# Optimization experiments

Hardware: AMD Instinct MI355X
Metric: run time of the kernel (lower is better)

## Reference

```python
import jax, jax.numpy as jnp
import numpy as np

B, C, N_MAX = 32, 1, 1024
HID, CLS, ATT_E, ATT_H = 128, 64, 64, 128
D = HID + CLS            # node_state_dim = hidden + class_repr
EDGE_F = 2 * ATT_E       # 128
K_MIX = 20
N_GNN = B * C * N_MAX    # 32768 GNN nodes
N_FEAT = N_GNN + 1       # node_feat rows after zero-pad row
E = 200_000
E_OUT = 500_000
NUM_SUB = 1024
NUM_PROP = 2             # num_GNN_prop (num_GNN_layers = 1)


def _lin(k, din, dout):
    k1, k2 = jax.random.split(k)
    s = 1.0 / np.sqrt(din)
    return (jax.random.uniform(k1, (din, dout), minval=-s, maxval=s),
            jax.random.uniform(k2, (dout,), minval=-s, maxval=s))


def setup_inputs() -> dict:
    key = jax.random.key(0)
    ks = jax.random.split(key, 30)
    inp = {}
    inp['A_pad'] = (jax.random.uniform(ks[0], (B, C, N_MAX, N_MAX)) < 0.05).astype(jnp.float32)
    inp['edges'] = jax.random.randint(ks[1], (E, 2), 0, N_GNN)
    inp['att_idx'] = jax.random.randint(ks[2], (N_GNN,), 0, ATT_E)
    inp['node_idx_feat'] = jax.random.randint(ks[3], (N_GNN,), 0, N_FEAT)
    inp['class_label'] = jax.random.randint(ks[4], (N_GNN,), 0, 2)
    inp['node_idx_gnn'] = jax.random.randint(ks[5], (E_OUT, 2), 0, N_GNN)
    inp['label'] = (jax.random.uniform(ks[6], (E_OUT,)) < 0.3).astype(jnp.float32)
    inp['subgraph_idx'] = jax.random.randint(ks[7], (E_OUT,), 0, NUM_SUB)
    # learned parameters
    inp['W_dec'], inp['b_dec'] = _lin(ks[8], N_MAX, HID)
    inp['class_emb'] = jax.random.normal(ks[9], (2, CLS)) * 0.1
    inp['W_msg1'], inp['b_msg1'] = _lin(ks[10], D + EDGE_F, D)
    inp['W_msg2'], inp['b_msg2'] = _lin(ks[11], D, D)
    inp['W_att1'], inp['b_att1'] = _lin(ks[12], D + EDGE_F, ATT_H)
    inp['W_att2'], inp['b_att2'] = _lin(ks[13], ATT_H, D)
    inp['W_ih'], inp['b_ih'] = _lin(ks[14], D, 3 * D)
    inp['W_hh'], inp['b_hh'] = _lin(ks[15], D, 3 * D)
    inp['Wt1'], inp['bt1'] = _lin(ks[16], D, HID)
    inp['Wt2'], inp['bt2'] = _lin(ks[17], HID, HID)
    inp['Wt3'], inp['bt3'] = _lin(ks[18], HID, K_MIX)
    inp['Wa1'], inp['ba1'] = _lin(ks[19], D, HID)
    inp['Wa2'], inp['ba2'] = _lin(ks[20], HID, HID)
    inp['Wa3'], inp['ba3'] = _lin(ks[21], HID, K_MIX)
    return inp


def _gran_forward(A_pad, label, W_dec, b_dec, class_emb,
                  W_msg1, b_msg1, W_msg2, b_msg2, W_att1, b_att1, W_att2, b_att2,
                  W_ih, b_ih, W_hh, b_hh, Wt1, bt1, Wt2, bt2, Wt3, bt3,
                  Wa1, ba1, Wa2, ba2, Wa3, ba3,
                  edges, att_idx, node_idx_feat, class_label, node_idx_gnn, subgraph_idx):
    # decoder_input: (B*C*N_max, N_max) -> hidden, then zero-pad one row on top
    A = A_pad.reshape(B * C * N_MAX, N_MAX)
    node_feat = A @ W_dec + b_dec                                   # [N_GNN, HID]
    node_feat = jnp.concatenate([jnp.zeros((1, HID), node_feat.dtype), node_feat], axis=0)
    # att_edge_feat: one-hot(att_idx[src]) || one-hot(att_idx[dst])  (scatter of ones)
    att_edge_feat = jnp.concatenate([
        jax.nn.one_hot(att_idx[edges[:, 0]], ATT_E, dtype=node_feat.dtype),
        jax.nn.one_hot(att_idx[edges[:, 1]], ATT_E, dtype=node_feat.dtype)], axis=1)  # [E, 128]
    # node state = gathered feat ++ class representation
    state = jnp.concatenate([node_feat[node_idx_feat], class_emb[class_label]], axis=1)  # [N_GNN, D]

    src, dst = edges[:, 0], edges[:, 1]

    def prop(state):
        diff = state[src] - state[dst]                              # gather node-diff [E, D]
        ei = jnp.concatenate([diff, att_edge_feat], axis=1)          # [E, D+128]
        msg = jax.nn.relu(ei @ W_msg1 + b_msg1) @ W_msg2 + b_msg2   # edge MLP [E, D]
        att = jax.nn.sigmoid(jax.nn.relu(ei @ W_att1 + b_att1) @ W_att2 + b_att2)
        agg = jax.ops.segment_sum(msg * att, dst, num_segments=N_GNN)  # scatter-add [N_GNN, D]
        # GRUCell(agg, state)
        gi = agg @ W_ih + b_ih
        gh = state @ W_hh + b_hh
        ir, iz, inn = jnp.split(gi, 3, axis=1)
        hr, hz, hn = jnp.split(gh, 3, axis=1)
        r = jax.nn.sigmoid(ir + hr)
        z = jax.nn.sigmoid(iz + hz)
        n = jnp.tanh(inn + r * hn)
        return (1.0 - z) * n + z * state

    for _ in range(NUM_PROP):
        state = prop(state)

    # output edge predictions from state diffs
    dout = state[node_idx_gnn[:, 0]] - state[node_idx_gnn[:, 1]]    # [E_OUT, D]
    h = jax.nn.relu(jax.nn.relu(dout @ Wt1 + bt1) @ Wt2 + bt2)
    log_theta = h @ Wt3 + bt3                                        # [E_OUT, K]
    g = jax.nn.relu(jax.nn.relu(dout @ Wa1 + ba1) @ Wa2 + ba2)
    log_alpha = jax.nn.log_softmax(g @ Wa3 + ba3, axis=1)            # [E_OUT, K]

    # mixture Bernoulli loss (BCEWithLogits, pos_weight=1): softplus(x) - x*y
    adj_loss = jax.nn.softplus(log_theta) - log_theta * label[:, None]
    const = jax.ops.segment_sum(jnp.ones((E_OUT,), log_theta.dtype), subgraph_idx, num_segments=NUM_SUB)
    const = jnp.maximum(const, 1.0)  # guard empty subgraphs with random indices
    red_loss = jax.ops.segment_sum(adj_loss, subgraph_idx, num_segments=NUM_SUB)
    red_alpha = jax.ops.segment_sum(log_alpha, subgraph_idx, num_segments=NUM_SUB) / const[:, None]
    log_prob = jax.nn.logsumexp(-red_loss + red_alpha, axis=1)       # [NUM_SUB]
    return -jnp.sum(log_prob) / float(E_OUT)


def reference(A_pad, edges, att_idx, node_idx_feat, class_label, node_idx_gnn, label, subgraph_idx,
              W_dec, b_dec, class_emb, W_msg1, b_msg1, W_msg2, b_msg2,
              W_att1, b_att1, W_att2, b_att2, W_ih, b_ih, W_hh, b_hh,
              Wt1, bt1, Wt2, bt2, Wt3, bt3, Wa1, ba1, Wa2, ba2, Wa3, ba3):
    return _gran_forward(A_pad, label, W_dec, b_dec, class_emb,
                         W_msg1, b_msg1, W_msg2, b_msg2, W_att1, b_att1, W_att2, b_att2,
                         W_ih, b_ih, W_hh, b_hh, Wt1, bt1, Wt2, bt2, Wt3, bt3,
                         Wa1, ba1, Wa2, ba2, Wa3, ba3,
                         edges, att_idx, node_idx_feat, class_label, node_idx_gnn, subgraph_idx)
```

## Files before the change

kernel.cpp:

```cpp
#include <hip/hip_runtime.h>
#include <math.h>

#define NGNN   32768
#define NMAXD  1024
#define HIDD   128
#define CLSD   64
#define DDIM   192
#define ATTH   128
#define NEDGE  200000
#define NEOUT  500000
#define NSUB   1024
#define KMIX   20

typedef __attribute__((ext_vector_type(8))) short bf16x8;
typedef __attribute__((ext_vector_type(8))) unsigned short u16x8;
typedef __attribute__((ext_vector_type(4))) float f32x4;

__device__ __forceinline__ float sigm(float x) { return 1.0f / (1.0f + __expf(-x)); }
__device__ __forceinline__ float tanhf_(float x) { return 2.0f / (1.0f + __expf(-2.0f * x)) - 1.0f; }

__device__ __forceinline__ short f2bf(float f) {
  union { float f; unsigned u; } v; v.f = f;
  unsigned r = v.u + 0x7FFFu + ((v.u >> 16) & 1u);
  return (short)(r >> 16);
}
__device__ __forceinline__ float bf2f(unsigned short u) {
  union { unsigned u; float f; } v; v.u = ((unsigned)u) << 16;
  return v.f;
}
__device__ __forceinline__ f32x4 bc4(float b) {
  f32x4 v; v[0] = b; v[1] = b; v[2] = b; v[3] = b; return v;
}

__global__ __launch_bounds__(64) void k_pack(const float* __restrict__ W,
                                             short* __restrict__ out, int N, int CT) {
  const int l = threadIdx.x;
  const int ks = blockIdx.x / CT;
  const int ct = blockIdx.x % CT;
  const int row0 = ks * 32 + (l >> 4) * 8;
  const int col = ct * 16 + (l & 15);
  short v[8];
#pragma unroll
  for (int j = 0; j < 8; j++) {
    const float f = (col < N) ? W[(size_t)(row0 + j) * N + col] : 0.0f;
    v[j] = f2bf(f);
  }
  *(bf16x8*)(out + ((size_t)blockIdx.x * 64 + l) * 8) = *(bf16x8*)v;
}

__global__ __launch_bounds__(128) void k_dec(
    const float* __restrict__ A, const float* __restrict__ Wd,
    const float* __restrict__ bd, float* __restrict__ nf) {
  __shared__ float arow[NMAXD];
  __shared__ int   nz[NMAXD];
  __shared__ int   cnt;
  const int row = blockIdx.x;
  const int t = threadIdx.x;
  if (t == 0) cnt = 0;
  const float4* A4 = (const float4*)(A + (size_t)row * NMAXD);
  float4* a4 = (float4*)arow;
  a4[t] = A4[t];
  a4[t + 128] = A4[t + 128];
  __syncthreads();
  for (int i = t; i < NMAXD; i += 128) {
    if (arow[i] != 0.0f) {
      int p = atomicAdd(&cnt, 1);
      nz[p] = i;
    }
  }
  __syncthreads();
  float acc = bd[t];
  const int n = cnt;
  for (int i = 0; i < n; i++) acc += Wd[(size_t)nz[i] * HIDD + t];
  nf[(size_t)row * HIDD + t] = acc;
}

__global__ __launch_bounds__(192) void k_state(
    const float* __restrict__ nf, const float* __restrict__ cemb,
    const int* __restrict__ nif, const int* __restrict__ cl,
    unsigned short* __restrict__ stbf) {
  const int i = blockIdx.x;
  const int t = threadIdx.x;
  float v;
  if (t < HIDD) {
    const int idx = nif[i];
    v = (idx == 0) ? 0.0f : nf[(size_t)(idx - 1) * HIDD + t];
  } else {
    v = cemb[cl[i] * CLSD + (t - HIDD)];
  }
  stbf[(size_t)i * DDIM + t] = (unsigned short)f2bf(v);
}

__global__ __launch_bounds__(128, 4) void k_edge_mfma(
    const unsigned short* __restrict__ stbf, const int* __restrict__ edges,
    const int* __restrict__ attidx,
    const float* __restrict__ Wm1, const float* __restrict__ bm1,
    const short* __restrict__ pWm1, const short* __restrict__ pWm2,
    const float* __restrict__ bm2,
    const float* __restrict__ Wa1, const float* __restrict__ ba1,
    const short* __restrict__ pWa1, const short* __restrict__ pWa2,
    const float* __restrict__ ba2,
    float* __restrict__ agg) {
  __shared__ short phm[6144];
  __shared__ short pha[4096];
  const int t = threadIdx.x;
  const int e0 = blockIdx.x * 32;
  const int wid = t >> 6, l = t & 63;
  const int col16 = l & 15, rr = (l >> 4) * 4;
  const int cb = (l >> 4) * 8;

  bf16x8 dfrag[6];
  {
    const int e = e0 + wid * 16 + (l & 15);
    const int s = edges[2 * e], d = edges[2 * e + 1];
    const unsigned short* ps = &stbf[(size_t)s * DDIM + cb];
    const unsigned short* pd_ = &stbf[(size_t)d * DDIM + cb];
#pragma unroll
    for (int ks = 0; ks < 6; ks++) {
      const u16x8 a = *(const u16x8*)(ps + ks * 32);
      const u16x8 b = *(const u16x8*)(pd_ + ks * 32);
      short v[8];
#pragma unroll
      for (int j = 0; j < 8; j++) v[j] = f2bf(bf2f(a[j]) - bf2f(b[j]));
      dfrag[ks] = *(bf16x8*)v;
    }
  }
  int a0r[4], a1r[4], dstr[4];
#pragma unroll
  for (int j = 0; j < 4; j++) {
    const int e = e0 + wid * 16 + rr + j;
    const int s = edges[2 * e], d = edges[2 * e + 1];
    a0r[j] = attidx[s]; a1r[j] = attidx[d]; dstr[j] = d;
  }

  for (int ct = 0; ct < 12; ct++) {
    const int col = ct * 16 + col16;
    f32x4 acc;
#pragma unroll
    for (int j = 0; j < 4; j++)
      acc[j] = bm1[col] + Wm1[(size_t)(DDIM + a0r[j]) * DDIM + col]
                        + Wm1[(size_t)(DDIM + 64 + a1r[j]) * DDIM + col];
#pragma unroll
    for (int ks = 0; ks < 6; ks++) {
      bf16x8 b = *(const bf16x8*)&pWm1[((ks * 12 + ct) * 64 + l) * 8];
      acc = __builtin_amdgcn_mfma_f32_16x16x32_bf16(dfrag[ks], b, acc, 0, 0, 0);
    }
    const int ksp = col >> 5, gp = (col & 31) >> 3, jp = col & 7;
#pragma unroll
    for (int j = 0; j < 4; j++)
      phm[((wid * 6 + ksp) * 64 + gp * 16 + rr + j) * 8 + jp] = f2bf(fmaxf(acc[j], 0.0f));
  }
  for (int ct = 0; ct < 8; ct++) {
    const int col = ct * 16 + col16;
    f32x4 acc;
#pragma unroll
    for (int j = 0; j < 4; j++)
      acc[j] = ba1[col] + Wa1[(size_t)(DDIM + a0r[j]) * ATTH + col]
                        + Wa1[(size_t)(DDIM + 64 + a1r[j]) * ATTH + col];
#pragma unroll
    for (int ks = 0; ks < 6; ks++) {
      bf16x8 b = *(const bf16x8*)&pWa1[((ks * 8 + ct) * 64 + l) * 8];
      acc = __builtin_amdgcn_mfma_f32_16x16x32_bf16(dfrag[ks], b, acc, 0, 0, 0);
    }
    const int ksp = ct >> 1, gp = ((ct & 1) * 16 + col16) >> 3, jp = col16 & 7;
#pragma unroll
    for (int j = 0; j < 4; j++)
      pha[((wid * 4 + ksp) * 64 + gp * 16 + rr + j) * 8 + jp] = f2bf(fmaxf(acc[j], 0.0f));
  }
  __syncthreads();

  for (int ct = 0; ct < 12; ct++) {
    const int col = ct * 16 + col16;
    f32x4 m = bc4(bm2[col]), av = bc4(ba2[col]);
#pragma unroll
    for (int ks = 0; ks < 6; ks++) {
      bf16x8 a = *(const bf16x8*)&phm[((wid * 6 + ks) * 64 + l) * 8];
      bf16x8 b = *(const bf16x8*)&pWm2[((ks * 12 + ct) * 64 + l) * 8];
      m = __builtin_amdgcn_mfma_f32_16x16x32_bf16(a, b, m, 0, 0, 0);
    }
#pragma unroll
    for (int ks = 0; ks < 4; ks++) {
      bf16x8 a = *(const bf16x8*)&pha[((wid * 4 + ks) * 64 + l) * 8];
      bf16x8 b = *(const bf16x8*)&pWa2[((ks * 12 + ct) * 64 + l) * 8];
      av = __builtin_amdgcn_mfma_f32_16x16x32_bf16(a, b, av, 0, 0, 0);
    }
#pragma unroll
    for (int j = 0; j < 4; j++) {
      atomicAdd(&agg[(size_t)dstr[j] * DDIM + col], m[j] * sigm(av[j]));
    }
  }
}

__global__ __launch_bounds__(256, 2) void k_gru_mfma(
    unsigned short* __restrict__ stbf, const float* __restrict__ agg,
    const short* __restrict__ pWih, const float* __restrict__ bih,
    const short* __restrict__ pWhh, const float* __restrict__ bhh) {
  const int t = threadIdx.x;
  const int n0 = blockIdx.x * 64;
  const int wid = t >> 6, l = t & 63;
  const int col16 = l & 15, rr = (l >> 4) * 4;
  const int cb = (l >> 4) * 8;
  const int row = n0 + wid * 16 + (l & 15);

  bf16x8 af[6], sf[6];
#pragma unroll
  for (int ks = 0; ks < 6; ks++) {
    const float4 a0 = *(const float4*)&agg[(size_t)row * DDIM + ks * 32 + cb];
    const float4 a1 = *(const float4*)&agg[(size_t)row * DDIM + ks * 32 + cb + 4];
    short v[8];
    v[0] = f2bf(a0.x); v[1] = f2bf(a0.y); v[2] = f2bf(a0.z); v[3] = f2bf(a0.w);
    v[4] = f2bf(a1.x); v[5] = f2bf(a1.y); v[6] = f2bf(a1.z); v[7] = f2bf(a1.w);
    af[ks] = *(bf16x8*)v;
    sf[ks] = *(const bf16x8*)&stbf[(size_t)row * DDIM + ks * 32 + cb];
  }

  for (int ct = 0; ct < 12; ct++) {
    const int c = ct * 16 + col16;
    f32x4 ir = bc4(bih[c]), iz = bc4(bih[c + DDIM]), in_ = bc4(bih[c + 2 * DDIM]);
    f32x4 hr = bc4(bhh[c]), hz = bc4(bhh[c + DDIM]), hn = bc4(bhh[c + 2 * DDIM]);
#pragma unroll
    for (int ks = 0; ks < 6; ks++) {
      const bf16x8 wr = *(const bf16x8*)&pWih[((size_t)(ks * 36 + ct) * 64 + l) * 8];
      const bf16x8 wz = *(const bf16x8*)&pWih[((size_t)(ks * 36 + ct + 12) * 64 + l) * 8];
      const bf16x8 wn = *(const bf16x8*)&pWih[((size_t)(ks * 36 + ct + 24) * 64 + l) * 8];
      ir  = __builtin_amdgcn_mfma_f32_16x16x32_bf16(af[ks], wr, ir, 0, 0, 0);
      iz  = __builtin_amdgcn_mfma_f32_16x16x32_bf16(af[ks], wz, iz, 0, 0, 0);
      in_ = __builtin_amdgcn_mfma_f32_16x16x32_bf16(af[ks], wn, in_, 0, 0, 0);
      const bf16x8 vr = *(const bf16x8*)&pWhh[((size_t)(ks * 36 + ct) * 64 + l) * 8];
      const bf16x8 vz = *(const bf16x8*)&pWhh[((size_t)(ks * 36 + ct + 12) * 64 + l) * 8];
      const bf16x8 vn = *(const bf16x8*)&pWhh[((size_t)(ks * 36 + ct + 24) * 64 + l) * 8];
      hr = __builtin_amdgcn_mfma_f32_16x16x32_bf16(sf[ks], vr, hr, 0, 0, 0);
      hz = __builtin_amdgcn_mfma_f32_16x16x32_bf16(sf[ks], vz, hz, 0, 0, 0);
      hn = __builtin_amdgcn_mfma_f32_16x16x32_bf16(sf[ks], vn, hn, 0, 0, 0);
    }
#pragma unroll
    for (int j = 0; j < 4; j++) {
      const size_t idx = (size_t)(n0 + wid * 16 + rr + j) * DDIM + c;
      const float sv = bf2f(stbf[idx]);
      const float r = sigm(ir[j] + hr[j]);
      const float z = sigm(iz[j] + hz[j]);
      const float nn = tanhf_(in_[j] + r * hn[j]);
      stbf[idx] = (unsigned short)f2bf((1.0f - z) * nn + z * sv);
    }
  }
}

__device__ __forceinline__ f32x4 head_branch(
    const bf16x8 dfrag[6], short* ph1, short* ph2,
    const short* __restrict__ pW1, const float* __restrict__ b1,
    const short* __restrict__ pW2, const float* __restrict__ b2,
    const short* __restrict__ pW3, const float* __restrict__ b3,
    int rt, int ch, int l) {
  const int col16 = l & 15, rr = (l >> 4) * 4;
  for (int ci = 0; ci < 4; ci++) {
    const int ct = ch * 4 + ci;
    const int col = ct * 16 + col16;
    f32x4 acc = bc4(b1[col]);
#pragma unroll
    for (int ks = 0; ks < 6; ks++) {
      bf16x8 b = *(const bf16x8*)&pW1[((ks * 8 + ct) * 64 + l) * 8];
      acc = __builtin_amdgcn_mfma_f32_16x16x32_bf16(dfrag[ks], b, acc, 0, 0, 0);
    }
    const int ksp = ct >> 1, gp = ((ct & 1) * 16 + col16) >> 3, jp = col16 & 7;
#pragma unroll
    for (int j = 0; j < 4; j++)
      ph1[((rt * 4 + ksp) * 64 + gp * 16 + rr + j) * 8 + jp] = f2bf(fmaxf(acc[j], 0.0f));
  }
  __syncthreads();
  for (int ci = 0; ci < 4; ci++) {
    const int ct = ch * 4 + ci;
    const int col = ct * 16 + col16;
    f32x4 acc = bc4(b2[col]);
#pragma unroll
    for (int ks = 0; ks < 4; ks++) {
      bf16x8 a = *(const bf16x8*)&ph1[((rt * 4 + ks) * 64 + l) * 8];
      bf16x8 b = *(const bf16x8*)&pW2[((ks * 8 + ct) * 64 + l) * 8];
      acc = __builtin_amdgcn_mfma_f32_16x16x32_bf16(a, b, acc, 0, 0, 0);
    }
    const int ksp = ct >> 1, gp = ((ct & 1) * 16 + col16) >> 3, jp = col16 & 7;
#pragma unroll
    for (int j = 0; j < 4; j++)
      ph2[((rt * 4 + ksp) * 64 + gp * 16 + rr + j) * 8 + jp] = f2bf(fmaxf(acc[j], 0.0f));
  }
  __syncthreads();
  const int col = ch * 16 + col16;
  f32x4 acc = bc4((col < KMIX) ? b3[col] : 0.0f);
#pragma unroll
  for (int ks = 0; ks < 4; ks++) {
    bf16x8 a = *(const bf16x8*)&ph2[((rt * 4 + ks) * 64 + l) * 8];
    bf16x8 b = *(const bf16x8*)&pW3[((ks * 2 + ch) * 64 + l) * 8];
    acc = __builtin_amdgcn_mfma_f32_16x16x32_bf16(a, b, acc, 0, 0, 0);
  }
  return acc;
}

__global__ __launch_bounds__(512, 4) void k_head_mfma(
    const unsigned short* __restrict__ stbf, const int* __restrict__ nig,
    const float* __restrict__ label, const int* __restrict__ subidx,
    const short* __restrict__ pWt1, const float* __restrict__ bt1,
    const short* __restrict__ pWt2, const float* __restrict__ bt2,
    const short* __restrict__ pWt3, const float* __restrict__ bt3,
    const short* __restrict__ pWa1, const float* __restrict__ ba1,
    const short* __restrict__ pWa2, const float* __restrict__ ba2,
    const short* __restrict__ pWa3, const float* __restrict__ ba3,
    float* __restrict__ red_loss, float* __restrict__ red_alpha,
    float* __restrict__ cnt) {
  __shared__ short ph1[8192];
  __shared__ short ph2[8192];
  __shared__ float la[64 * KMIX];
  __shared__ int   ssub[64];
  __shared__ float slab[64];
  __shared__ float lse[64];

  const int t = threadIdx.x;
  const int r0 = blockIdx.x * 64;

  if (t < 64) {
    const int gr = r0 + t;
    const int sb = (gr < NEOUT) ? subidx[gr] : 0;
    ssub[t] = sb;
    slab[t] = (gr < NEOUT) ? label[gr] : 0.0f;
    if (gr < NEOUT) atomicAdd(&cnt[sb], 1.0f);
  }

  const int wid = t >> 6, l = t & 63;
  const int rt = wid & 3, ch = wid >> 2;
  const int col16 = l & 15, rr = (l >> 4) * 4;
  const int cb = (l >> 4) * 8;

  bf16x8 dfrag[6];
  {
    const int gr = r0 + rt * 16 + (l & 15);
    const int ok = (gr < NEOUT);
    const int ia = ok ? nig[2 * gr] : 0;
    const int ib = ok ? nig[2 * gr + 1] : 0;
    const unsigned short* pa = &stbf[(size_t)ia * DDIM + cb];
    const unsigned short* pb = &stbf[(size_t)ib * DDIM + cb];
#pragma unroll
    for (int ks = 0; ks < 6; ks++) {
      const u16x8 a = *(const u16x8*)(pa + ks * 32);
      const u16x8 b = *(const u16x8*)(pb + ks * 32);
      short v[8];
#pragma unroll
      for (int j = 0; j < 8; j++) v[j] = f2bf(bf2f(a[j]) - bf2f(b[j]));
      dfrag[ks] = *(bf16x8*)v;
    }
  }
  __syncthreads();

  {
    const f32x4 o = head_branch(dfrag, ph1, ph2, pWt1, bt1, pWt2, bt2, pWt3, bt3, rt, ch, l);
    const int col = ch * 16 + col16;
    if (col < KMIX) {
#pragma unroll
      for (int j = 0; j < 4; j++) {
        const int r = rt * 16 + rr + j;
        if (r0 + r < NEOUT) {
          const float lt = o[j];
          const float adj = fmaxf(lt, 0.0f) + logf(1.0f + __expf(-fabsf(lt))) - lt * slab[r];
          atomicAdd(&red_loss[ssub[r] * KMIX + col], adj);
        }
      }
    }
  }
  __syncthreads();
  {
    const f32x4 o = head_branch(dfrag, ph1, ph2, pWa1, ba1, pWa2, ba2, pWa3, ba3, rt, ch, l);
    const int col = ch * 16 + col16;
    if (col < KMIX) {
#pragma unroll
      for (int j = 0; j < 4; j++) {
        const int r = rt * 16 + rr + j;
        la[r * KMIX + col] = o[j];
      }
    }
  }
  __syncthreads();
  if (t < 64) {
    float m = -1e30f;
    for (int k = 0; k < KMIX; k++) m = fmaxf(m, la[t * KMIX + k]);
    float s = 0.0f;
    for (int k = 0; k < KMIX; k++) s += __expf(la[t * KMIX + k] - m);
    lse[t] = m + logf(s);
  }
  __syncthreads();
  {
    const int r = t >> 3;
    if (r0 + r < NEOUT) {
#pragma unroll
      for (int i = 0; i < 3; i++) {
        const int c = (t & 7) + 8 * i;
        if (c < KMIX)
          atomicAdd(&red_alpha[ssub[r] * KMIX + c], la[r * KMIX + c] - lse[r]);
      }
    }
  }
}

__global__ __launch_bounds__(1024) void k_final(
    const float* __restrict__ red_loss, const float* __restrict__ red_alpha,
    const float* __restrict__ cnt, float* __restrict__ out) {
  __shared__ float part[1024];
  const int s = threadIdx.x;
  const float c = fmaxf(cnt[s], 1.0f);
  float v[KMIX];
  float m = -1e30f;
  for (int k = 0; k < KMIX; k++) {
    v[k] = -red_loss[s * KMIX + k] + red_alpha[s * KMIX + k] / c;
    m = fmaxf(m, v[k]);
  }
  float sum = 0.0f;
  for (int k = 0; k < KMIX; k++) sum += __expf(v[k] - m);
  part[s] = m + logf(sum);
  __syncthreads();
  for (int st = 512; st > 0; st >>= 1) {
    if (s < st) part[s] += part[s + st];
    __syncthreads();
  }
  if (s == 0) out[0] = -part[0] / (float)NEOUT;
}

extern "C" void kernel_launch(void* const* d_in, const int* in_sizes, int n_in,
                              void* d_out, int out_size, void* d_ws, size_t ws_size,
                              hipStream_t stream) {
  const float* A      = (const float*)d_in[0];
  const int*   edges  = (const int*)d_in[1];
  const int*   attidx = (const int*)d_in[2];
  const int*   nif    = (const int*)d_in[3];
  const int*   cl     = (const int*)d_in[4];
  const int*   nig    = (const int*)d_in[5];
  const float* label  = (const float*)d_in[6];
  const int*   subidx = (const int*)d_in[7];
  const float* Wdec   = (const float*)d_in[8];
  const float* bdec   = (const float*)d_in[9];
  const float* cemb   = (const float*)d_in[10];
  const float* Wm1    = (const float*)d_in[11];
  const float* bm1    = (const float*)d_in[12];
  const float* Wm2    = (const float*)d_in[13];
  const float* bm2    = (const float*)d_in[14];
  const float* Wa1    = (const float*)d_in[15];
  const float* ba1    = (const float*)d_in[16];
  const float* Wa2    = (const float*)d_in[17];
  const float* ba2    = (const float*)d_in[18];
  const float* Wih    = (const float*)d_in[19];
  const float* bih    = (const float*)d_in[20];
  const float* Whh    = (const float*)d_in[21];
  const float* bhh    = (const float*)d_in[22];
  const float* Wt1    = (const float*)d_in[23];
  const float* bt1    = (const float*)d_in[24];
  const float* Wt2    = (const float*)d_in[25];
  const float* bt2    = (const float*)d_in[26];
  const float* Wt3    = (const float*)d_in[27];
  const float* bt3    = (const float*)d_in[28];
  const float* Wha1   = (const float*)d_in[29];
  const float* hba1   = (const float*)d_in[30];
  const float* Wha2   = (const float*)d_in[31];
  const float* hba2   = (const float*)d_in[32];
  const float* Wha3   = (const float*)d_in[33];
  const float* hba3   = (const float*)d_in[34];

  char* ws = (char*)d_ws;
  const size_t SZ_STBF = (size_t)NGNN * DDIM * sizeof(short);
  const size_t SZ_AGG  = (size_t)NGNN * DDIM * sizeof(float);
  unsigned short* stbf = (unsigned short*)ws;
  float* agg       = (float*)(ws + SZ_STBF);
  float* nf        = agg;
  float* red_loss  = (float*)(ws + SZ_STBF + SZ_AGG);
  float* red_alpha = red_loss + NSUB * KMIX;
  float* cnt       = red_alpha + NSUB * KMIX;
  short* pk        = (short*)(ws + SZ_STBF + SZ_AGG +
                              (((size_t)(2 * NSUB * KMIX + NSUB) * 4 + 255) / 256) * 256);
  short* pWm1  = pk;
  short* pWa1e = pWm1  + 36864;
  short* pWm2  = pWa1e + 24576;
  short* pWa2e = pWm2  + 36864;
  short* pWt1  = pWa2e + 24576;
  short* pWt2  = pWt1  + 24576;
  short* pWt3  = pWt2  + 16384;
  short* pWh1  = pWt3  + 4096;
  short* pWh2  = pWh1  + 24576;
  short* pWh3  = pWh2  + 16384;
  short* pWih  = pWh3  + 4096;
  short* pWhh  = pWih  + 110592;

  k_pack<<<72, 64, 0, stream>>>(Wm1,  pWm1,  192, 12);
  k_pack<<<48, 64, 0, stream>>>(Wa1,  pWa1e, 128, 8);
  k_pack<<<72, 64, 0, stream>>>(Wm2,  pWm2,  192, 12);
  k_pack<<<48, 64, 0, stream>>>(Wa2,  pWa2e, 192, 12);
  k_pack<<<48, 64, 0, stream>>>(Wt1,  pWt1,  128, 8);
  k_pack<<<32, 64, 0, stream>>>(Wt2,  pWt2,  128, 8);
  k_pack<<< 8, 64, 0, stream>>>(Wt3,  pWt3,   20, 2);
  k_pack<<<48, 64, 0, stream>>>(Wha1, pWh1,  128, 8);
  k_pack<<<32, 64, 0, stream>>>(Wha2, pWh2,  128, 8);
  k_pack<<< 8, 64, 0, stream>>>(Wha3, pWh3,   20, 2);
  k_pack<<<216, 64, 0, stream>>>(Wih, pWih,  576, 36);
  k_pack<<<216, 64, 0, stream>>>(Whh, pWhh,  576, 36);

  k_dec<<<NGNN, 128, 0, stream>>>(A, Wdec, bdec, nf);
  k_state<<<NGNN, 192, 0, stream>>>(nf, cemb, nif, cl, stbf);
  for (int p = 0; p < 2; p++) {
    hipMemsetAsync(agg, 0, SZ_AGG, stream);
    k_edge_mfma<<<NEDGE / 32, 128, 0, stream>>>(stbf, edges, attidx,
        Wm1, bm1, pWm1, pWm2, bm2, Wa1, ba1, pWa1e, pWa2e, ba2, agg);
    k_gru_mfma<<<NGNN / 64, 256, 0, stream>>>(stbf, agg, pWih, bih, pWhh, bhh);
  }
  hipMemsetAsync(red_loss, 0, (size_t)(2 * NSUB * KMIX + NSUB) * sizeof(float), stream);
  k_head_mfma<<<(NEOUT + 63) / 64, 512, 0, stream>>>(stbf, nig, label, subidx,
      pWt1, bt1, pWt2, bt2, pWt3, bt3, pWh1, hba1, pWh2, hba2, pWh3, hba3,
      red_loss, red_alpha, cnt);
  k_final<<<1, 1024, 0, stream>>>(red_loss, red_alpha, cnt, (float*)d_out);
}
```

Before: 986.6 us.

## Replicate head reduction buffers and interleave theta/alpha MLP branches

The segment-sum accumulators for loss, alpha and counts are now spread across 64 replicas chosen by block index, and a new k_red kernel sums them before k_final. This is meant to cut atomic contention on the 1024x20 subgraph buckets. The two head MLP branches are also computed together in one pass with separate LDS buffers, which halves the number of barriers and gives the scheduler two independent MFMA chains. The costs are doubled LDS use (occupancy drops to 2 blocks per CU), a larger memset and one extra kernel launch.

```diff
diff --git a/kernel.cpp b/kernel.cpp
--- a/kernel.cpp
+++ b/kernel.cpp
@@ -11,6 +11,12 @@
 #define NEOUT  500000
 #define NSUB   1024
 #define KMIX   20
+
+#define NREP      64
+#define LOSS_OFF  0
+#define ALPHA_OFF 20480
+#define CNT_OFF   40960
+#define REP_STRIDE 41984
 
 typedef __attribute__((ext_vector_type(8))) short bf16x8;
 typedef __attribute__((ext_vector_type(8))) unsigned short u16x8;
@@ -245,56 +251,7 @@
   }
 }
 
-__device__ __forceinline__ f32x4 head_branch(
-    const bf16x8 dfrag[6], short* ph1, short* ph2,
-    const short* __restrict__ pW1, const float* __restrict__ b1,
-    const short* __restrict__ pW2, const float* __restrict__ b2,
-    const short* __restrict__ pW3, const float* __restrict__ b3,
-    int rt, int ch, int l) {
-  const int col16 = l & 15, rr = (l >> 4) * 4;
-  for (int ci = 0; ci < 4; ci++) {
-    const int ct = ch * 4 + ci;
-    const int col = ct * 16 + col16;
-    f32x4 acc = bc4(b1[col]);
-#pragma unroll
-    for (int ks = 0; ks < 6; ks++) {
-      bf16x8 b = *(const bf16x8*)&pW1[((ks * 8 + ct) * 64 + l) * 8];
-      acc = __builtin_amdgcn_mfma_f32_16x16x32_bf16(dfrag[ks], b, acc, 0, 0, 0);
-    }
-    const int ksp = ct >> 1, gp = ((ct & 1) * 16 + col16) >> 3, jp = col16 & 7;
-#pragma unroll
-    for (int j = 0; j < 4; j++)
-      ph1[((rt * 4 + ksp) * 64 + gp * 16 + rr + j) * 8 + jp] = f2bf(fmaxf(acc[j], 0.0f));
-  }
-  __syncthreads();
-  for (int ci = 0; ci < 4; ci++) {
-    const int ct = ch * 4 + ci;
-    const int col = ct * 16 + col16;
-    f32x4 acc = bc4(b2[col]);
-#pragma unroll
-    for (int ks = 0; ks < 4; ks++) {
-      bf16x8 a = *(const bf16x8*)&ph1[((rt * 4 + ks) * 64 + l) * 8];
-      bf16x8 b = *(const bf16x8*)&pW2[((ks * 8 + ct) * 64 + l) * 8];
-      acc = __builtin_amdgcn_mfma_f32_16x16x32_bf16(a, b, acc, 0, 0, 0);
-    }
-    const int ksp = ct >> 1, gp = ((ct & 1) * 16 + col16) >> 3, jp = col16 & 7;
-#pragma unroll
-    for (int j = 0; j < 4; j++)
-      ph2[((rt * 4 + ksp) * 64 + gp * 16 + rr + j) * 8 + jp] = f2bf(fmaxf(acc[j], 0.0f));
-  }
-  __syncthreads();
-  const int col = ch * 16 + col16;
-  f32x4 acc = bc4((col < KMIX) ? b3[col] : 0.0f);
-#pragma unroll
-  for (int ks = 0; ks < 4; ks++) {
-    bf16x8 a = *(const bf16x8*)&ph2[((rt * 4 + ks) * 64 + l) * 8];
-    bf16x8 b = *(const bf16x8*)&pW3[((ks * 2 + ch) * 64 + l) * 8];
-    acc = __builtin_amdgcn_mfma_f32_16x16x32_bf16(a, b, acc, 0, 0, 0);
-  }
-  return acc;
-}
-
-__global__ __launch_bounds__(512, 4) void k_head_mfma(
+__global__ __launch_bounds__(512, 2) void k_head_mfma(
     const unsigned short* __restrict__ stbf, const int* __restrict__ nig,
     const float* __restrict__ label, const int* __restrict__ subidx,
     const short* __restrict__ pWt1, const float* __restrict__ bt1,
@@ -303,10 +260,9 @@
     const short* __restrict__ pWa1, const float* __restrict__ ba1,
     const short* __restrict__ pWa2, const float* __restrict__ ba2,
     const short* __restrict__ pWa3, const float* __restrict__ ba3,
-    float* __restrict__ red_loss, float* __restrict__ red_alpha,
-    float* __restrict__ cnt) {
-  __shared__ short ph1[8192];
-  __shared__ short ph2[8192];
+    float* __restrict__ REP) {
+  __shared__ short ph1t[8192], ph1a[8192];
+  __shared__ short ph2t[8192], ph2a[8192];
   __shared__ float la[64 * KMIX];
   __shared__ int   ssub[64];
   __shared__ float slab[64];
@@ -314,13 +270,14 @@
 
   const int t = threadIdx.x;
   const int r0 = blockIdx.x * 64;
+  float* rep = REP + (size_t)(blockIdx.x & (NREP - 1)) * REP_STRIDE;
 
   if (t < 64) {
     const int gr = r0 + t;
     const int sb = (gr < NEOUT) ? subidx[gr] : 0;
     ssub[t] = sb;
     slab[t] = (gr < NEOUT) ? label[gr] : 0.0f;
-    if (gr < NEOUT) atomicAdd(&cnt[sb], 1.0f);
+    if (gr < NEOUT) atomicAdd(&rep[CNT_OFF + sb], 1.0f);
   }
 
   const int wid = t >> 6, l = t & 63;
@@ -346,33 +303,74 @@
       dfrag[ks] = *(bf16x8*)v;
     }
   }
-  __syncthreads();
-
-  {
-    const f32x4 o = head_branch(dfrag, ph1, ph2, pWt1, bt1, pWt2, bt2, pWt3, bt3, rt, ch, l);
-    const int col = ch * 16 + col16;
-    if (col < KMIX) {
-#pragma unroll
-      for (int j = 0; j < 4; j++) {
-        const int r = rt * 16 + rr + j;
-        if (r0 + r < NEOUT) {
-          const float lt = o[j];
-          const float adj = fmaxf(lt, 0.0f) + logf(1.0f + __expf(-fabsf(lt))) - lt * slab[r];
-          atomicAdd(&red_loss[ssub[r] * KMIX + col], adj);
-        }
+
+  for (int ci = 0; ci < 4; ci++) {
+    const int ct = ch * 4 + ci;
+    const int col = ct * 16 + col16;
+    f32x4 at = bc4(bt1[col]), aa = bc4(ba1[col]);
+#pragma unroll
+    for (int ks = 0; ks < 6; ks++) {
+      bf16x8 b1 = *(const bf16x8*)&pWt1[((ks * 8 + ct) * 64 + l) * 8];
+      bf16x8 b2 = *(const bf16x8*)&pWa1[((ks * 8 + ct) * 64 + l) * 8];
+      at = __builtin_amdgcn_mfma_f32_16x16x32_bf16(dfrag[ks], b1, at, 0, 0, 0);
+      aa = __builtin_amdgcn_mfma_f32_16x16x32_bf16(dfrag[ks], b2, aa, 0, 0, 0);
+    }
+    const int ksp = ct >> 1, gp = ((ct & 1) * 16 + col16) >> 3, jp = col16 & 7;
+#pragma unroll
+    for (int j = 0; j < 4; j++) {
+      const int o = ((rt * 4 + ksp) * 64 + gp * 16 + rr + j) * 8 + jp;
+      ph1t[o] = f2bf(fmaxf(at[j], 0.0f));
+      ph1a[o] = f2bf(fmaxf(aa[j], 0.0f));
+    }
+  }
+  __syncthreads();
+  for (int ci = 0; ci < 4; ci++) {
+    const int ct = ch * 4 + ci;
+    const int col = ct * 16 + col16;
+    f32x4 at = bc4(bt2[col]), aa = bc4(ba2[col]);
+#pragma unroll
+    for (int ks = 0; ks < 4; ks++) {
+      const int ao = ((rt * 4 + ks) * 64 + l) * 8;
+      bf16x8 a1 = *(const bf16x8*)&ph1t[ao];
+      bf16x8 a2 = *(const bf16x8*)&ph1a[ao];
+      bf16x8 b1 = *(const bf16x8*)&pWt2[((ks * 8 + ct) * 64 + l) * 8];
+      bf16x8 b2 = *(const bf16x8*)&pWa2[((ks * 8 + ct) * 64 + l) * 8];
+      at = __builtin_amdgcn_mfma_f32_16x16x32_bf16(a1, b1, at, 0, 0, 0);
+      aa = __builtin_amdgcn_mfma_f32_16x16x32_bf16(a2, b2, aa, 0, 0, 0);
+    }
+    const int ksp = ct >> 1, gp = ((ct & 1) * 16 + col16) >> 3, jp = col16 & 7;
+#pragma unroll
+    for (int j = 0; j < 4; j++) {
+      const int o = ((rt * 4 + ksp) * 64 + gp * 16 + rr + j) * 8 + jp;
+      ph2t[o] = f2bf(fmaxf(at[j], 0.0f));
+      ph2a[o] = f2bf(fmaxf(aa[j], 0.0f));
+    }
+  }
+  __syncthreads();
+  const int col = ch * 16 + col16;
+  f32x4 ot = bc4((col < KMIX) ? bt3[col] : 0.0f);
+  f32x4 oa = bc4((col < KMIX) ? ba3[col] : 0.0f);
+#pragma unroll
+  for (int ks = 0; ks < 4; ks++) {
+    const int ao = ((rt * 4 + ks) * 64 + l) * 8;
+    bf16x8 a1 = *(const bf16x8*)&ph2t[ao];
+    bf16x8 a2 = *(const bf16x8*)&ph2a[ao];
+    bf16x8 b1 = *(const bf16x8*)&pWt3[((ks * 2 + ch) * 64 + l) * 8];
+    bf16x8 b2 = *(const bf16x8*)&pWa3[((ks * 2 + ch) * 64 + l) * 8];
+    ot = __builtin_amdgcn_mfma_f32_16x16x32_bf16(a1, b1, ot, 0, 0, 0);
+    oa = __builtin_amdgcn_mfma_f32_16x16x32_bf16(a2, b2, oa, 0, 0, 0);
+  }
+
+  if (col < KMIX) {
+#pragma unroll
+    for (int j = 0; j < 4; j++) {
+      const int r = rt * 16 + rr + j;
+      if (r0 + r < NEOUT) {
+        const float lt = ot[j];
+        const float adj = fmaxf(lt, 0.0f) + logf(1.0f + __expf(-fabsf(lt))) - lt * slab[r];
+        atomicAdd(&rep[LOSS_OFF + ssub[r] * KMIX + col], adj);
       }
-    }
-  }
-  __syncthreads();
-  {
-    const f32x4 o = head_branch(dfrag, ph1, ph2, pWa1, ba1, pWa2, ba2, pWa3, ba3, rt, ch, l);
-    const int col = ch * 16 + col16;
-    if (col < KMIX) {
-#pragma unroll
-      for (int j = 0; j < 4; j++) {
-        const int r = rt * 16 + rr + j;
-        la[r * KMIX + col] = o[j];
-      }
+      la[(rt * 16 + rr + j) * KMIX + col] = oa[j];
     }
   }
   __syncthreads();
@@ -391,18 +389,29 @@
       for (int i = 0; i < 3; i++) {
         const int c = (t & 7) + 8 * i;
         if (c < KMIX)
-          atomicAdd(&red_alpha[ssub[r] * KMIX + c], la[r * KMIX + c] - lse[r]);
+          atomicAdd(&rep[ALPHA_OFF + ssub[r] * KMIX + c], la[r * KMIX + c] - lse[r]);
       }
     }
   }
 }
 
+__global__ __launch_bounds__(256) void k_red(const float* __restrict__ REP,
+                                             float* __restrict__ fin) {
+  const int i = blockIdx.x * 256 + threadIdx.x;
+  if (i < REP_STRIDE) {
+    float s = 0.0f;
+    for (int r = 0; r < NREP; r++) s += REP[(size_t)r * REP_STRIDE + i];
+    fin[i] = s;
+  }
+}
+
 __global__ __launch_bounds__(1024) void k_final(
-    const float* __restrict__ red_loss, const float* __restrict__ red_alpha,
-    const float* __restrict__ cnt, float* __restrict__ out) {
+    const float* __restrict__ fin, float* __restrict__ out) {
   __shared__ float part[1024];
   const int s = threadIdx.x;
-  const float c = fmaxf(cnt[s], 1.0f);
+  const float* red_loss  = fin + LOSS_OFF;
+  const float* red_alpha = fin + ALPHA_OFF;
+  const float c = fmaxf(fin[CNT_OFF + s], 1.0f);
   float v[KMIX];
   float m = -1e30f;
   for (int k = 0; k < KMIX; k++) {
@@ -462,14 +471,14 @@
   char* ws = (char*)d_ws;
   const size_t SZ_STBF = (size_t)NGNN * DDIM * sizeof(short);
   const size_t SZ_AGG  = (size_t)NGNN * DDIM * sizeof(float);
+  const size_t SZ_REP  = (size_t)NREP * REP_STRIDE * sizeof(float);
   unsigned short* stbf = (unsigned short*)ws;
   float* agg       = (float*)(ws + SZ_STBF);
   float* nf        = agg;
-  float* red_loss  = (float*)(ws + SZ_STBF + SZ_AGG);
-  float* red_alpha = red_loss + NSUB * KMIX;
-  float* cnt       = red_alpha + NSUB * KMIX;
-  short* pk        = (short*)(ws + SZ_STBF + SZ_AGG +
-                              (((size_t)(2 * NSUB * KMIX + NSUB) * 4 + 255) / 256) * 256);
+  float* REP       = (float*)(ws + SZ_STBF + SZ_AGG);
+  float* fin       = (float*)(ws + SZ_STBF + SZ_AGG + SZ_REP);
+  short* pk        = (short*)(ws + SZ_STBF + SZ_AGG + SZ_REP +
+                              (((size_t)REP_STRIDE * 4 + 255) / 256) * 256);
   short* pWm1  = pk;
   short* pWa1e = pWm1  + 36864;
   short* pWm2  = pWa1e + 24576;
@@ -504,9 +513,9 @@
         Wm1, bm1, pWm1, pWm2, bm2, Wa1, ba1, pWa1e, pWa2e, ba2, agg);
     k_gru_mfma<<<NGNN / 64, 256, 0, stream>>>(stbf, agg, pWih, bih, pWhh, bhh);
   }
-  hipMemsetAsync(red_loss, 0, (size_t)(2 * NSUB * KMIX + NSUB) * sizeof(float), stream);
+  hipMemsetAsync(REP, 0, SZ_REP, stream);
   k_head_mfma<<<(NEOUT + 63) / 64, 512, 0, stream>>>(stbf, nig, label, subidx,
-      pWt1, bt1, pWt2, bt2, pWt3, bt3, pWh1, hba1, pWh2, hba2, pWh3, hba3,
-      red_loss, red_alpha, cnt);
-  k_final<<<1, 1024, 0, stream>>>(red_loss, red_alpha, cnt, (float*)d_out);
-}
+      pWt1, bt1, pWt2, bt2, pWt3, bt3, pWh1, hba1, pWh2, hba2, pWh3, hba3, REP);
+  k_red<<<(REP_STRIDE + 255) / 256, 256, 0, stream>>>(REP, fin);
+  k_final<<<1, 1024, 0, stream>>>(fin, (float*)d_out);
+}
```

Measured after the change: 962.7 us. -2.4%, faster.
